# Kernel tuning notes

Measured on AMD Instinct MI355X. Metric: run time of the kernel, lower is better.

Reference implementation:

```python
import jax, jax.numpy as jnp
import numpy as np

H = 768        # bert hidden_size
HID = 512      # lstm_hidden
HALF = HID // 2
T = 20         # tagset_size
START, STOP = 18, 19
S = 16386      # input positions incl. CLS/SEP
NEG = -10000.0


def setup_inputs() -> dict:
    key = jax.random.key(0)
    ks = jax.random.split(key, 12)
    sc_x = 1.0
    x = jax.random.normal(ks[0], (1, S, H), dtype=jnp.float32)
    # PyTorch LSTM params (gate order i,f,g,o), one layer, bidirectional
    s_ih = 1.0 / np.sqrt(HALF)
    w_ih_f = jax.random.uniform(ks[1], (4 * HALF, H), jnp.float32, -s_ih, s_ih)
    w_hh_f = jax.random.uniform(ks[2], (4 * HALF, HALF), jnp.float32, -s_ih, s_ih)
    b_ih_f = jax.random.uniform(ks[3], (4 * HALF,), jnp.float32, -s_ih, s_ih)
    b_hh_f = jax.random.uniform(ks[4], (4 * HALF,), jnp.float32, -s_ih, s_ih)
    w_ih_b = jax.random.uniform(ks[5], (4 * HALF, H), jnp.float32, -s_ih, s_ih)
    w_hh_b = jax.random.uniform(ks[6], (4 * HALF, HALF), jnp.float32, -s_ih, s_ih)
    b_ih_b = jax.random.uniform(ks[7], (4 * HALF,), jnp.float32, -s_ih, s_ih)
    b_hh_b = jax.random.uniform(ks[8], (4 * HALF,), jnp.float32, -s_ih, s_ih)
    s_t = 1.0 / np.sqrt(HID)
    w_tag = jax.random.uniform(ks[9], (T, HID), jnp.float32, -s_t, s_t)
    b_tag = jax.random.uniform(ks[10], (T,), jnp.float32, -s_t, s_t)
    transitions = jax.random.normal(ks[11], (T, T), dtype=jnp.float32)
    transitions = transitions.at[START, :].set(NEG).at[:, STOP].set(NEG)
    return {
        "x": x,
        "w_ih_f": w_ih_f, "w_hh_f": w_hh_f, "b_ih_f": b_ih_f, "b_hh_f": b_hh_f,
        "w_ih_b": w_ih_b, "w_hh_b": w_hh_b, "b_ih_b": b_ih_b, "b_hh_b": b_hh_b,
        "w_tag": w_tag, "b_tag": b_tag, "transitions": transitions,
    }


def _lstm_one_step(xt, w_ih, b_ih, b_hh):
    # Original passes [1, N, H] to a batch_first=False LSTM => seq_len=1,
    # batch=N, zero initial state. So each token does ONE cell step:
    # h0=c0=0 => hh contribution is only b_hh.
    g = xt @ w_ih.T + b_ih + b_hh          # [N, 4*HALF]
    i, f, gg, o = jnp.split(g, 4, axis=-1)  # PyTorch gate order i,f,g,o
    c = jax.nn.sigmoid(i) * jnp.tanh(gg)    # f*c0 = 0
    return jax.nn.sigmoid(o) * jnp.tanh(c)  # [N, HALF]


def reference(x, w_ih_f, w_hh_f, b_ih_f, b_hh_f,
              w_ih_b, w_hh_b, b_ih_b, b_hh_b,
              w_tag, b_tag, transitions):
    tok = x[0, 1:-1, :]                     # narrow(1,1,S-2): drop CLS/SEP -> [N,H]
    h_f = _lstm_one_step(tok, w_ih_f, b_ih_f, b_hh_f)
    h_b = _lstm_one_step(tok, w_ih_b, b_ih_b, b_hh_b)
    enc = jnp.concatenate([h_f, h_b], axis=-1)   # [N, HID]
    feats = enc @ w_tag.T + b_tag                # [N, T] emission scores

    # ---- Viterbi decode (sequential DP over tokens) ----
    init = jnp.full((T,), NEG, dtype=feats.dtype).at[START].set(0.0)

    def vstep(fv, feat):
        scores = fv[None, :] + transitions       # [next_tag, prev_tag]
        bp = jnp.argmax(scores, axis=1)          # backpointers [T]
        fv_new = jnp.max(scores, axis=1) + feat
        return fv_new, bp

    fv, bps = jax.lax.scan(vstep, init, feats)   # bps: [N, T]
    terminal = fv + transitions[STOP]
    best = jnp.argmax(terminal)
    path_score = terminal[best]

    def btrack(b, bp):
        return bp[b], b                          # emit tag at time t, move to t-1

    _, best_path = jax.lax.scan(btrack, best, bps, reverse=True)  # [N] in time order
    return path_score, best_path
```

## Files before the change

### kernel.cpp

```cpp
#include <hip/hip_runtime.h>
#include <math.h>

#define HDIM 768
#define HIDD 512
#define NTOK 16384
#define NT 20
#define CHUNKS 128
#define CLEN 128

typedef unsigned short ushort_t;
typedef __attribute__((ext_vector_type(8))) short bf16x8;
typedef __attribute__((ext_vector_type(4))) float f32x4;

__device__ __forceinline__ float sigm(float x){ return 1.0f/(1.0f+expf(-x)); }

__device__ __forceinline__ ushort_t f2bf(float f){
    unsigned int u = __float_as_uint(f);
    unsigned int r = (u + 0x7fffu + ((u >> 16) & 1u)) >> 16;
    return (ushort_t)r;
}
__device__ __forceinline__ float bf2f(ushort_t b){
    return __uint_as_float(((unsigned int)b) << 16);
}

#define GLD16(gp, lp) __builtin_amdgcn_global_load_lds( \
    (const __attribute__((address_space(1))) void*)(gp), \
    (__attribute__((address_space(3))) void*)(lp), 16, 0, 0)

__global__ __launch_bounds__(256) void conv_kernel(
    const float* __restrict__ x,
    const float* __restrict__ wf, const float* __restrict__ wb,
    ushort_t* __restrict__ Ah, ushort_t* __restrict__ Al,
    ushort_t* __restrict__ Bh, ushort_t* __restrict__ Bl)
{
    const int bid = blockIdx.x;
    if (bid < 1152){
        int t = bid*256 + threadIdx.x;
        int n = t / 192, c4 = (t - n*192)*4;
        int dir = n / 768, nr = n - dir*768;
        int gate = nr >> 8, j = nr & 255;
        int wrow = j + ((gate==0)?0:((gate==1)?512:768));
        const float* src = dir ? wb : wf;
        const float4 v = *(const float4*)(src + (size_t)wrow*HDIM + c4);
        float f[4] = {v.x, v.y, v.z, v.w};
        ushort_t h[4], l[4];
        #pragma unroll
        for (int i=0;i<4;++i){
            h[i] = f2bf(f[i]);
            l[i] = f2bf(f[i] - bf2f(h[i]));
        }
        *(ushort4*)(Bh + (size_t)n*HDIM + c4) = make_ushort4(h[0],h[1],h[2],h[3]);
        *(ushort4*)(Bl + (size_t)n*HDIM + c4) = make_ushort4(l[0],l[1],l[2],l[3]);
    } else {
        int t = (bid-1152)*256 + threadIdx.x;
        int row = t / 192, c4 = (t - row*192)*4;
        const float4 v = *(const float4*)(x + (size_t)(row+1)*HDIM + c4);
        float f[4] = {v.x, v.y, v.z, v.w};
        ushort_t h[4], l[4];
        #pragma unroll
        for (int i=0;i<4;++i){
            h[i] = f2bf(f[i]);
            l[i] = f2bf(f[i] - bf2f(h[i]));
        }
        *(ushort4*)(Ah + (size_t)row*HDIM + c4) = make_ushort4(h[0],h[1],h[2],h[3]);
        *(ushort4*)(Al + (size_t)row*HDIM + c4) = make_ushort4(l[0],l[1],l[2],l[3]);
    }
}

#define VMCNT(n) asm volatile("s_waitcnt vmcnt(" #n ")" ::: "memory")
#define BARRIER() asm volatile("s_barrier" ::: "memory")

#define READ_B(S, g, ab) do{                                                  \
    bfr##S[0] = *(const bf16x8*)((ab) + 16384 + (g)*16384 + boffB[0]);        \
    bfr##S[1] = *(const bf16x8*)((ab) + 16384 + (g)*16384 + 8192 + boffB[0]); \
    bfr##S[2] = *(const bf16x8*)((ab) + 16384 + (g)*16384 + boffB[1]);        \
    bfr##S[3] = *(const bf16x8*)((ab) + 16384 + (g)*16384 + 8192 + boffB[1]); \
}while(0)

#define READ_A2(S, ab) do{ _Pragma("unroll") for (int f=0; f<4; ++f){         \
    aH##S[f] = *(const bf16x8*)((ab) + aoffB[f]);                             \
    aL##S[f] = *(const bf16x8*)((ab) + 8192 + aoffB[f]); } }while(0)

#define MFMA_CLUSTER(g, AS, BS) do{                                           \
  __builtin_amdgcn_sched_barrier(0);                                          \
  __builtin_amdgcn_s_setprio(1);                                              \
  _Pragma("unroll")                                                           \
  for (int fn=0; fn<2; ++fn){                                                 \
    _Pragma("unroll")                                                         \
    for (int fm=0; fm<4; ++fm){                                               \
      acc[g][fm][fn] = __builtin_amdgcn_mfma_f32_16x16x32_bf16(aH##AS[fm],    \
          bfr##BS[fn*2], acc[g][fm][fn], 0, 0, 0);                            \
      acc[g][fm][fn] = __builtin_amdgcn_mfma_f32_16x16x32_bf16(aL##AS[fm],    \
          bfr##BS[fn*2], acc[g][fm][fn], 0, 0, 0);                            \
      acc[g][fm][fn] = __builtin_amdgcn_mfma_f32_16x16x32_bf16(aH##AS[fm],    \
          bfr##BS[fn*2+1], acc[g][fm][fn], 0, 0, 0);                          \
    }                                                                         \
  }                                                                           \
  __builtin_amdgcn_s_setprio(0);                                              \
  __builtin_amdgcn_sched_barrier(0);                                          \
}while(0)

#define PH0(kt, P, AC, BC, BR) do{                                            \
    const int k0n = ((kt)+1)*32;                                              \
    char* abn = smem + (1-(P))*65536;                                         \
    const char* ab = smem + (P)*65536;                                        \
    VMCNT(2); BARRIER();                                                      \
    READ_B(BR, 1, ab);                                                        \
    GLD16(Ah + gA + k0n, abn + wbB);                                          \
    GLD16(Al + gA + k0n, abn + 8192 + wbB);                                   \
    GLD16(Bh + gB0 + k0n, abn + 16384 + wbB);                                 \
    GLD16(Bl + gB0 + k0n, abn + 24576 + wbB);                                 \
    MFMA_CLUSTER(0, AC, BC);                                                  \
}while(0)

#define PH1(kt, P, AC, BC, BR) do{                                            \
    const int k0n = ((kt)+1)*32;                                              \
    char* abn = smem + (1-(P))*65536;                                         \
    const char* ab = smem + (P)*65536;                                        \
    VMCNT(4); BARRIER();                                                      \
    READ_B(BR, 2, ab);                                                        \
    GLD16(Bh + gB1 + k0n, abn + 32768 + wbB);                                 \
    GLD16(Bl + gB1 + k0n, abn + 40960 + wbB);                                 \
    MFMA_CLUSTER(1, AC, BC);                                                  \
}while(0)

#define PH2(kt, P, AC, BC, BR, AN) do{                                        \
    const int k0n = ((kt)+1)*32;                                              \
    char* abn = smem + (1-(P))*65536;                                         \
    VMCNT(2); BARRIER();                                                      \
    READ_A2(AN, abn);                                                         \
    READ_B(BR, 0, abn);                                                       \
    GLD16(Bh + gB2 + k0n, abn + 49152 + wbB);                                 \
    GLD16(Bl + gB2 + k0n, abn + 57344 + wbB);                                 \
    MFMA_CLUSTER(2, AC, BC);                                                  \
}while(0)

__global__ __launch_bounds__(512, 2) void gemm_fused(
    const ushort_t* __restrict__ Ah, const ushort_t* __restrict__ Al,
    const ushort_t* __restrict__ Bh, const ushort_t* __restrict__ Bl,
    const float* __restrict__ bihf, const float* __restrict__ bhhf,
    const float* __restrict__ bihb, const float* __restrict__ bhhb,
    const float* __restrict__ wtag, float* __restrict__ featsp)
{
    __shared__ __align__(16) char smem[131072];
    float* hbuf = (float*)smem;
    float* wts  = (float*)(smem + 33280);

    const int tid = threadIdx.x;
    const int bx = blockIdx.x;
    const int xcd = bx & 7, g3 = bx >> 3;
    const int qb = g3 & 3, mt = (g3 >> 2)*8 + xcd;
    const int dir = qb >> 1, jhalf = qb & 1;
    const int j0 = jhalf*128;
    const int row0 = mt*128;
    const float* __restrict__ bih = dir ? bihb : bihf;
    const float* __restrict__ bhh = dir ? bhhb : bhhf;

    const int lane = tid & 63, wv = tid >> 6;
    const int wm = wv >> 2, wn = wv & 3;
    const int lm = lane & 15, lq = lane >> 4;
    const int wbB = (tid & 448) * 16;

    const int P_ = tid >> 3, s_ = tid & 7;
    const int q_ = s_ ^ (P_ & 7);
    const int mA = (P_ << 1) | (q_ >> 2);
    const int k8s = q_ & 3;
    const size_t gA  = (size_t)(row0 + mA)*HDIM + k8s*8;
    const size_t gB0 = (size_t)(dir*768 +           j0 + mA)*HDIM + k8s*8;
    const size_t gB1 = (size_t)(dir*768 + 256 +     j0 + mA)*HDIM + k8s*8;
    const size_t gB2 = (size_t)(dir*768 + 512 +     j0 + mA)*HDIM + k8s*8;

    int aoffB[4], boffB[2];
    #pragma unroll
    for (int f=0; f<4; ++f){
        int m = wm*64 + f*16 + lm;
        int rg = m >> 6, r = m & 63;
        aoffB[f] = rg*4096 + ((r>>1)*8 + ((((r&1)<<2)|lq) ^ ((r>>1)&7)))*16;
    }
    #pragma unroll
    for (int f=0; f<2; ++f){
        int n = wn*32 + f*16 + lm;
        int rg = n >> 6, r = n & 63;
        boffB[f] = rg*4096 + ((r>>1)*8 + ((((r&1)<<2)|lq) ^ ((r>>1)&7)))*16;
    }

    f32x4 acc[3][4][2];
    #pragma unroll
    for (int g=0; g<3; ++g)
        #pragma unroll
        for (int fm=0; fm<4; ++fm)
            #pragma unroll
            for (int fn=0; fn<2; ++fn)
                acc[g][fm][fn] = (f32x4){0.f,0.f,0.f,0.f};

    bf16x8 aH0[4], aL0[4], aH1[4], aL1[4];
    bf16x8 bfrA[4], bfrB[4];

    {
        GLD16(Ah + gA, smem + wbB);
        GLD16(Al + gA, smem + 8192 + wbB);
        GLD16(Bh + gB0, smem + 16384 + wbB);
        GLD16(Bl + gB0, smem + 24576 + wbB);
        GLD16(Bh + gB1, smem + 32768 + wbB);
        GLD16(Bl + gB1, smem + 40960 + wbB);
        GLD16(Bh + gB2, smem + 49152 + wbB);
        GLD16(Bl + gB2, smem + 57344 + wbB);
        VMCNT(4); BARRIER();
        READ_A2(0, (const char*)smem);
        READ_B(A, 0, (const char*)smem);
    }

    #pragma unroll 1
    for (int kt2 = 0; kt2 < 11; ++kt2){
        const int kt = kt2*2;
        PH0(kt,   0, 0, A, B); PH1(kt,   0, 0, B, A); PH2(kt,   0, 0, A, B, 1);
        PH0(kt+1, 1, 1, B, A); PH1(kt+1, 1, 1, A, B); PH2(kt+1, 1, 1, B, A, 0);
    }
    PH0(22, 0, 0, A, B); PH1(22, 0, 0, B, A); PH2(22, 0, 0, A, B, 1);

    {
        const char* ab = smem + 65536;
        VMCNT(2); BARRIER();
        READ_B(A, 1, ab);
        MFMA_CLUSTER(0, 1, B);
        VMCNT(0); BARRIER();
        READ_B(B, 2, ab);
        MFMA_CLUSTER(1, 1, A);
        MFMA_CLUSTER(2, 1, B);
    }

    int jcol[2];
    #pragma unroll
    for (int f=0; f<2; ++f) jcol[f] = j0 + wn*32 + f*16 + lm;

    float bi[2], bg_[2], bo[2];
    #pragma unroll
    for (int f=0; f<2; ++f){
        bi[f]  = bih[jcol[f]]       + bhh[jcol[f]];
        bg_[f] = bih[512 + jcol[f]] + bhh[512 + jcol[f]];
        bo[f]  = bih[768 + jcol[f]] + bhh[768 + jcol[f]];
    }
    float hv[4][2][4];
    #pragma unroll
    for (int fm=0; fm<4; ++fm)
        #pragma unroll
        for (int fn=0; fn<2; ++fn)
            #pragma unroll
            for (int r=0; r<4; ++r){
                float cv = sigm(acc[0][fm][fn][r] + bi[fn]) *
                           tanhf(acc[1][fm][fn][r] + bg_[fn]);
                hv[fm][fn][r] = sigm(acc[2][fm][fn][r] + bo[fn]) * tanhf(cv);
            }

    __syncthreads();
    for (int idx=tid; idx<2*NT*64; idx+=512){
        int cc = idx / (NT*64), r = idx - cc*(NT*64);
        int t = r >> 6, j = r & 63;
        wts[idx] = wtag[t*HIDD + dir*256 + j0 + cc*64 + j];
    }
    #pragma unroll 1
    for (int cc=0; cc<2; ++cc){
        __syncthreads();
        if ((wn >> 1) == cc){
            #pragma unroll
            for (int fm=0; fm<4; ++fm)
                #pragma unroll
                for (int fn=0; fn<2; ++fn)
                    #pragma unroll
                    for (int r=0; r<4; ++r){
                        int mloc = wm*64 + fm*16 + lq*4 + r;
                        int jloc = (wn&1)*32 + fn*16 + lm;
                        hbuf[mloc*65 + jloc] = hv[fm][fn][r];
                    }
        }
        __syncthreads();
        const int mrow = tid & 127, grp = tid >> 7;
        const int tg0 = grp*5;
        const float* wc = wts + cc*(NT*64);
        float s[5] = {0.f,0.f,0.f,0.f,0.f};
        for (int j=0;j<64;++j){
            float h = hbuf[mrow*65 + j];
            #pragma unroll
            for (int tt=0; tt<5; ++tt)
                s[tt] = fmaf(h, wc[(tg0+tt)*64 + j], s[tt]);
        }
        const int p = dir*4 + jhalf*2 + cc;
        float* fq = featsp + (size_t)p * (NTOK*NT);
        const int mglob = row0 + mrow;
        #pragma unroll
        for (int tt=0; tt<5; ++tt)
            fq[(size_t)mglob*NT + tg0 + tt] = s[tt];
    }
}

__device__ __forceinline__ void load_fl(
    const float* __restrict__ featsp, const float* __restrict__ btg,
    float* fl, int c, int tid, int nthr)
{
    const int base = c*(CLEN*NT/4);
    for (int idx=tid; idx<CLEN*NT/4; idx+=nthr){
        float4 s[8];
        #pragma unroll
        for (int p=0; p<8; ++p)
            s[p] = ((const float4*)(featsp + (size_t)p*NTOK*NT))[base+idx];
        float4 v;
        v.x = ((s[0].x+s[1].x)+(s[2].x+s[3].x)) + ((s[4].x+s[5].x)+(s[6].x+s[7].x));
        v.y = ((s[0].y+s[1].y)+(s[2].y+s[3].y)) + ((s[4].y+s[5].y)+(s[6].y+s[7].y));
        v.z = ((s[0].z+s[1].z)+(s[2].z+s[3].z)) + ((s[4].z+s[5].z)+(s[6].z+s[7].z));
        v.w = ((s[0].w+s[1].w)+(s[2].w+s[3].w)) + ((s[4].w+s[5].w)+(s[6].w+s[7].w));
        int t0 = (idx*4) % 20;
        v.x += btg[t0]; v.y += btg[t0+1]; v.z += btg[t0+2]; v.w += btg[t0+3];
        ((float4*)fl)[idx] = v;
    }
}

__global__ __launch_bounds__(256) void vit_chunkmat(
    const float* __restrict__ featsp, const float* __restrict__ btag,
    const float* __restrict__ trans, float* __restrict__ Pall)
{
    __shared__ float fl[CLEN*NT];
    __shared__ float Pt[2][NT*24];
    const int c = blockIdx.x, tid = threadIdx.x;
    load_fl(featsp, btag, fl, c, tid, 256);
    const bool act = tid < 200;
    const int j = tid / 10, ip = tid - j*10;
    const int ia = ip*2, ib = ia + 1;
    float tra[NT], trb[NT];
    if (act){
        #pragma unroll
        for (int k=0;k<NT;++k){
            tra[k] = trans[ia*NT+k];
            trb[k] = trans[ib*NT+k];
        }
        Pt[0][j*24+ia] = (ia==j) ? 0.f : -1e30f;
        Pt[0][j*24+ib] = (ib==j) ? 0.f : -1e30f;
    }
    __syncthreads();
    int cur = 0;
    #pragma unroll 1
    for (int t=0;t<CLEN;++t){
        if (act){
            float p[NT];
            #pragma unroll
            for (int q=0;q<5;++q){
                float4 v = *(const float4*)&Pt[cur][j*24 + q*4];
                p[q*4+0]=v.x; p[q*4+1]=v.y; p[q*4+2]=v.z; p[q*4+3]=v.w;
            }
            float ma = -3.0e38f, mb = -3.0e38f;
            #pragma unroll
            for (int k=0;k<NT;++k){
                ma = fmaxf(ma, tra[k] + p[k]);
                mb = fmaxf(mb, trb[k] + p[k]);
            }
            ma += fl[t*NT+ia];
            mb += fl[t*NT+ib];
            Pt[cur^1][j*24+ia] = ma;
            Pt[cur^1][j*24+ib] = mb;
        }
        __syncthreads();
        cur ^= 1;
    }
    if (act){
        Pall[(size_t)c*(NT*NT) + ia*NT + j] = Pt[cur][j*24+ia];
        Pall[(size_t)c*(NT*NT) + ib*NT + j] = Pt[cur][j*24+ib];
    }
}

__global__ __launch_bounds__(128) void vit_scan(
    const float* __restrict__ Pall, const float* __restrict__ trans,
    float* __restrict__ fvstart, float* __restrict__ dout, int* __restrict__ bestws)
{
    __shared__ float Pb[NT*NT];
    __shared__ float fv[NT];
    const int tid = threadIdx.x;
    float4 pn = {0.f,0.f,0.f,0.f};
    if (tid<100) pn = ((const float4*)Pall)[tid];
    if (tid<NT) fv[tid] = (tid==18) ? 0.f : -10000.f;
    for (int c=0;c<CHUNKS;++c){
        if (tid<100) ((float4*)Pb)[tid] = pn;
        if (tid<100 && c+1<CHUNKS) pn = ((const float4*)(Pall + (size_t)(c+1)*(NT*NT)))[tid];
        __syncthreads();
        if (tid<NT) fvstart[c*NT+tid] = fv[tid];
        float nf = -3.0e38f;
        if (tid<NT){
            #pragma unroll
            for (int j=0;j<NT;++j) nf = fmaxf(nf, Pb[tid*NT+j] + fv[j]);
        }
        __syncthreads();
        if (tid<NT) fv[tid] = nf;
    }
    __syncthreads();
    if (tid==0){
        float best = -3.0e38f; int bidx = 0;
        for (int j=0;j<NT;++j){
            float tv = fv[j] + trans[19*NT+j];
            if (tv > best){ best = tv; bidx = j; }
        }
        dout[0] = best;
        bestws[0] = bidx;
    }
}

__global__ __launch_bounds__(128) void vit_replay(
    const float* __restrict__ featsp, const float* __restrict__ btag,
    const float* __restrict__ trans, const float* __restrict__ fvstart,
    unsigned int* __restrict__ bpout, int* __restrict__ Hout)
{
    __shared__ float fl[CLEN*NT];
    __shared__ float fv[NT];
    __shared__ unsigned char bp[CLEN*NT];
    const int c = blockIdx.x, tid = threadIdx.x;
    load_fl(featsp, btag, fl, c, tid, 128);
    float tr[NT];
    if (tid<NT){
        fv[tid] = fvstart[c*NT+tid];
        #pragma unroll
        for (int k=0;k<NT;++k) tr[k] = trans[tid*NT+k];
    }
    __syncthreads();
    for (int t=0;t<CLEN;++t){
        float best = 0.f; int bj = 0;
        if (tid<NT){
            best = tr[0] + fv[0];
            #pragma unroll
            for (int j=1;j<NT;++j){
                float v = tr[j] + fv[j];
                if (v > best){ best = v; bj = j; }
            }
        }
        __syncthreads();
        if (tid<NT){
            fv[tid] = best + fl[t*NT+tid];
            bp[t*NT+tid] = (unsigned char)bj;
        }
        __syncthreads();
    }
    for (int idx=tid; idx<CLEN*NT/4; idx+=128)
        bpout[(size_t)c*(CLEN*NT/4) + idx] = ((unsigned int*)bp)[idx];
    if (tid<NT){
        int m = tid;
        for (int t=CLEN-1;t>=0;--t) m = bp[t*NT+m];
        Hout[c*NT+tid] = m;
    }
}

__global__ __launch_bounds__(64) void bt_fill(
    const unsigned int* __restrict__ bpin, const int* __restrict__ Hin,
    const int* __restrict__ bestws, float* __restrict__ dout)
{
    __shared__ int Hl[CHUNKS*NT];
    __shared__ unsigned char bp[CLEN*NT];
    __shared__ float ob[CLEN];
    const int c = blockIdx.x, tid = threadIdx.x;
    for (int idx=tid; idx<CHUNKS*NT; idx+=64) Hl[idx] = Hin[idx];
    for (int idx=tid; idx<CLEN*NT/4; idx+=64)
        ((unsigned int*)bp)[idx] = bpin[(size_t)c*(CLEN*NT/4) + idx];
    __syncthreads();
    if (tid==0){
        int e = bestws[0];
        for (int cc=CHUNKS-1; cc>c; --cc) e = Hl[cc*NT+e];
        for (int t=CLEN-1;t>=0;--t){ ob[t] = (float)e; e = bp[t*NT+e]; }
    }
    __syncthreads();
    for (int idx=tid; idx<CLEN; idx+=64)
        dout[1 + c*CLEN + idx] = ob[idx];
}

extern "C" void kernel_launch(void* const* d_in, const int* in_sizes, int n_in,
                              void* d_out, int out_size, void* d_ws, size_t ws_size,
                              hipStream_t stream)
{
    const float* x    = (const float*)d_in[0];
    const float* wf   = (const float*)d_in[1];
    const float* bihf = (const float*)d_in[3];
    const float* bhhf = (const float*)d_in[4];
    const float* wb   = (const float*)d_in[5];
    const float* bihb = (const float*)d_in[7];
    const float* bhhb = (const float*)d_in[8];
    const float* wtag = (const float*)d_in[9];
    const float* btag = (const float*)d_in[10];
    const float* trans= (const float*)d_in[11];
    float* out = (float*)d_out;

    char* w = (char*)d_ws;
    ushort_t* Ah = (ushort_t*)w;         w += 25165824;
    ushort_t* Al = (ushort_t*)w;         w += 25165824;
    ushort_t* Bh = (ushort_t*)w;         w += 2359296;
    ushort_t* Bl = (ushort_t*)w;         w += 2359296;
    float* featsp = (float*)w;           w += 10485760;
    float* Pall  = (float*)w;            w += 204800;
    float* fvst  = (float*)w;            w += 10240;
    int* Hmap    = (int*)w;              w += 10240;
    unsigned int* bp = (unsigned int*)w; w += 327680;
    int* best    = (int*)w;

    conv_kernel<<<13440, 256, 0, stream>>>(x, wf, wb, Ah, Al, Bh, Bl);
    gemm_fused<<<512, 512, 0, stream>>>(Ah, Al, Bh, Bl, bihf, bhhf, bihb, bhhb,
                                        wtag, featsp);
    vit_chunkmat<<<CHUNKS, 256, 0, stream>>>(featsp, btag, trans, Pall);
    vit_scan<<<1, 128, 0, stream>>>(Pall, trans, fvst, out, best);
    vit_replay<<<CHUNKS, 128, 0, stream>>>(featsp, btag, trans, fvst, bp, Hmap);
    bt_fill<<<CHUNKS, 64, 0, stream>>>(bp, Hmap, best, out);
}
```

Baseline: 366.9 us.

## Load GEMM B operand directly from global into registers, shrink LDS

The B (weight) fragments are now loaded straight from global memory into a register double buffer for the next k-step, instead of being staged through LDS with swizzled layouts. Only the A tile stays in LDS, so shared memory drops from 128KB to about 43KB and the per-phase barriers collapse into one wait-and-barrier per k-step. The aim is to cut LDS traffic and barrier count and to raise occupancy headroom. In exchange there are uncoalesced per-lane global reads of B, which are duplicated across the waves sharing a column slice, plus 24 extra bf16x8 registers. The full VMCNT(0) wait each step also removes the finer-grained overlap of the old schedule.

Result: slower. 503.1 us (+37.1%).

```diff
diff --git a/kernel.cpp b/kernel.cpp
--- a/kernel.cpp
+++ b/kernel.cpp
@@ -70,69 +70,48 @@
 #define VMCNT(n) asm volatile("s_waitcnt vmcnt(" #n ")" ::: "memory")
 #define BARRIER() asm volatile("s_barrier" ::: "memory")
 
-#define READ_B(S, g, ab) do{                                                  \
-    bfr##S[0] = *(const bf16x8*)((ab) + 16384 + (g)*16384 + boffB[0]);        \
-    bfr##S[1] = *(const bf16x8*)((ab) + 16384 + (g)*16384 + 8192 + boffB[0]); \
-    bfr##S[2] = *(const bf16x8*)((ab) + 16384 + (g)*16384 + boffB[1]);        \
-    bfr##S[3] = *(const bf16x8*)((ab) + 16384 + (g)*16384 + 8192 + boffB[1]); \
+#define LOADB(S, KT) do{                                                      \
+  _Pragma("unroll")                                                           \
+  for (int g=0; g<3; ++g)                                                     \
+    _Pragma("unroll")                                                         \
+    for (int f=0; f<2; ++f){                                                  \
+      bs##S[g*4+f*2+0] = *(const bf16x8*)((const char*)Bh + bByte[g][f] + (KT)*64); \
+      bs##S[g*4+f*2+1] = *(const bf16x8*)((const char*)Bl + bByte[g][f] + (KT)*64); \
+    }                                                                         \
 }while(0)
 
-#define READ_A2(S, ab) do{ _Pragma("unroll") for (int f=0; f<4; ++f){         \
-    aH##S[f] = *(const bf16x8*)((ab) + aoffB[f]);                             \
-    aL##S[f] = *(const bf16x8*)((ab) + 8192 + aoffB[f]); } }while(0)
-
-#define MFMA_CLUSTER(g, AS, BS) do{                                           \
+#define READ_A(ab) do{ _Pragma("unroll") for (int f=0; f<4; ++f){             \
+    aH[f] = *(const bf16x8*)((ab) + aoffB[f]);                                \
+    aL[f] = *(const bf16x8*)((ab) + 8192 + aoffB[f]); } }while(0)
+
+#define MFMA_CLUSTER(g, S) do{                                                \
   __builtin_amdgcn_sched_barrier(0);                                          \
   __builtin_amdgcn_s_setprio(1);                                              \
   _Pragma("unroll")                                                           \
   for (int fn=0; fn<2; ++fn){                                                 \
     _Pragma("unroll")                                                         \
     for (int fm=0; fm<4; ++fm){                                               \
-      acc[g][fm][fn] = __builtin_amdgcn_mfma_f32_16x16x32_bf16(aH##AS[fm],    \
-          bfr##BS[fn*2], acc[g][fm][fn], 0, 0, 0);                            \
-      acc[g][fm][fn] = __builtin_amdgcn_mfma_f32_16x16x32_bf16(aL##AS[fm],    \
-          bfr##BS[fn*2], acc[g][fm][fn], 0, 0, 0);                            \
-      acc[g][fm][fn] = __builtin_amdgcn_mfma_f32_16x16x32_bf16(aH##AS[fm],    \
-          bfr##BS[fn*2+1], acc[g][fm][fn], 0, 0, 0);                          \
+      acc[g][fm][fn] = __builtin_amdgcn_mfma_f32_16x16x32_bf16(aH[fm],        \
+          bs##S[(g)*4+fn*2], acc[g][fm][fn], 0, 0, 0);                        \
+      acc[g][fm][fn] = __builtin_amdgcn_mfma_f32_16x16x32_bf16(aL[fm],        \
+          bs##S[(g)*4+fn*2], acc[g][fm][fn], 0, 0, 0);                        \
+      acc[g][fm][fn] = __builtin_amdgcn_mfma_f32_16x16x32_bf16(aH[fm],        \
+          bs##S[(g)*4+fn*2+1], acc[g][fm][fn], 0, 0, 0);                      \
     }                                                                         \
   }                                                                           \
   __builtin_amdgcn_s_setprio(0);                                              \
   __builtin_amdgcn_sched_barrier(0);                                          \
 }while(0)
 
-#define PH0(kt, P, AC, BC, BR) do{                                            \
-    const int k0n = ((kt)+1)*32;                                              \
-    char* abn = smem + (1-(P))*65536;                                         \
-    const char* ab = smem + (P)*65536;                                        \
-    VMCNT(2); BARRIER();                                                      \
-    READ_B(BR, 1, ab);                                                        \
-    GLD16(Ah + gA + k0n, abn + wbB);                                          \
-    GLD16(Al + gA + k0n, abn + 8192 + wbB);                                   \
-    GLD16(Bh + gB0 + k0n, abn + 16384 + wbB);                                 \
-    GLD16(Bl + gB0 + k0n, abn + 24576 + wbB);                                 \
-    MFMA_CLUSTER(0, AC, BC);                                                  \
-}while(0)
-
-#define PH1(kt, P, AC, BC, BR) do{                                            \
-    const int k0n = ((kt)+1)*32;                                              \
-    char* abn = smem + (1-(P))*65536;                                         \
-    const char* ab = smem + (P)*65536;                                        \
-    VMCNT(4); BARRIER();                                                      \
-    READ_B(BR, 2, ab);                                                        \
-    GLD16(Bh + gB1 + k0n, abn + 32768 + wbB);                                 \
-    GLD16(Bl + gB1 + k0n, abn + 40960 + wbB);                                 \
-    MFMA_CLUSTER(1, AC, BC);                                                  \
-}while(0)
-
-#define PH2(kt, P, AC, BC, BR, AN) do{                                        \
-    const int k0n = ((kt)+1)*32;                                              \
-    char* abn = smem + (1-(P))*65536;                                         \
-    VMCNT(2); BARRIER();                                                      \
-    READ_A2(AN, abn);                                                         \
-    READ_B(BR, 0, abn);                                                       \
-    GLD16(Bh + gB2 + k0n, abn + 49152 + wbB);                                 \
-    GLD16(Bl + gB2 + k0n, abn + 57344 + wbB);                                 \
-    MFMA_CLUSTER(2, AC, BC);                                                  \
+#define KT_BODY(KT, P, CUR, NXT) do{                                          \
+    VMCNT(0); BARRIER();                                                      \
+    READ_A(smem + (P)*16384);                                                 \
+    LOADB(NXT, (KT)+1);                                                       \
+    GLD16(Ah + gA + ((KT)+1)*32, smem + (1-(P))*16384 + wbB);                 \
+    GLD16(Al + gA + ((KT)+1)*32, smem + (1-(P))*16384 + 8192 + wbB);          \
+    MFMA_CLUSTER(0, CUR);                                                     \
+    MFMA_CLUSTER(1, CUR);                                                     \
+    MFMA_CLUSTER(2, CUR);                                                     \
 }while(0)
 
 __global__ __launch_bounds__(512, 2) void gemm_fused(
@@ -142,7 +121,7 @@
     const float* __restrict__ bihb, const float* __restrict__ bhhb,
     const float* __restrict__ wtag, float* __restrict__ featsp)
 {
-    __shared__ __align__(16) char smem[131072];
+    __shared__ __align__(16) char smem[43520];
     float* hbuf = (float*)smem;
     float* wts  = (float*)(smem + 33280);
 
@@ -166,23 +145,22 @@
     const int mA = (P_ << 1) | (q_ >> 2);
     const int k8s = q_ & 3;
     const size_t gA  = (size_t)(row0 + mA)*HDIM + k8s*8;
-    const size_t gB0 = (size_t)(dir*768 +           j0 + mA)*HDIM + k8s*8;
-    const size_t gB1 = (size_t)(dir*768 + 256 +     j0 + mA)*HDIM + k8s*8;
-    const size_t gB2 = (size_t)(dir*768 + 512 +     j0 + mA)*HDIM + k8s*8;
-
-    int aoffB[4], boffB[2];
+
+    int aoffB[4];
     #pragma unroll
     for (int f=0; f<4; ++f){
         int m = wm*64 + f*16 + lm;
         int rg = m >> 6, r = m & 63;
         aoffB[f] = rg*4096 + ((r>>1)*8 + ((((r&1)<<2)|lq) ^ ((r>>1)&7)))*16;
     }
-    #pragma unroll
-    for (int f=0; f<2; ++f){
-        int n = wn*32 + f*16 + lm;
-        int rg = n >> 6, r = n & 63;
-        boffB[f] = rg*4096 + ((r>>1)*8 + ((((r&1)<<2)|lq) ^ ((r>>1)&7)))*16;
-    }
+
+    int bByte[3][2];
+    #pragma unroll
+    for (int g=0; g<3; ++g)
+        #pragma unroll
+        for (int f=0; f<2; ++f)
+            bByte[g][f] = (dir*768 + g*256 + j0 + wn*32 + f*16 + lm)*(HDIM*2)
+                          + lq*16;
 
     f32x4 acc[3][4][2];
     #pragma unroll
@@ -193,40 +171,26 @@
             for (int fn=0; fn<2; ++fn)
                 acc[g][fm][fn] = (f32x4){0.f,0.f,0.f,0.f};
 
-    bf16x8 aH0[4], aL0[4], aH1[4], aL1[4];
-    bf16x8 bfrA[4], bfrB[4];
-
-    {
-        GLD16(Ah + gA, smem + wbB);
-        GLD16(Al + gA, smem + 8192 + wbB);
-        GLD16(Bh + gB0, smem + 16384 + wbB);
-        GLD16(Bl + gB0, smem + 24576 + wbB);
-        GLD16(Bh + gB1, smem + 32768 + wbB);
-        GLD16(Bl + gB1, smem + 40960 + wbB);
-        GLD16(Bh + gB2, smem + 49152 + wbB);
-        GLD16(Bl + gB2, smem + 57344 + wbB);
-        VMCNT(4); BARRIER();
-        READ_A2(0, (const char*)smem);
-        READ_B(A, 0, (const char*)smem);
-    }
+    bf16x8 aH[4], aL[4];
+    bf16x8 bsA[12], bsB[12];
+
+    LOADB(A, 0);
+    GLD16(Ah + gA, smem + wbB);
+    GLD16(Al + gA, smem + 8192 + wbB);
 
     #pragma unroll 1
     for (int kt2 = 0; kt2 < 11; ++kt2){
-        const int kt = kt2*2;
-        PH0(kt,   0, 0, A, B); PH1(kt,   0, 0, B, A); PH2(kt,   0, 0, A, B, 1);
-        PH0(kt+1, 1, 1, B, A); PH1(kt+1, 1, 1, A, B); PH2(kt+1, 1, 1, B, A, 0);
-    }
-    PH0(22, 0, 0, A, B); PH1(22, 0, 0, B, A); PH2(22, 0, 0, A, B, 1);
+        KT_BODY(2*kt2,   0, A, B);
+        KT_BODY(2*kt2+1, 1, B, A);
+    }
+    KT_BODY(22, 0, A, B);
 
     {
-        const char* ab = smem + 65536;
-        VMCNT(2); BARRIER();
-        READ_B(A, 1, ab);
-        MFMA_CLUSTER(0, 1, B);
         VMCNT(0); BARRIER();
-        READ_B(B, 2, ab);
-        MFMA_CLUSTER(1, 1, A);
-        MFMA_CLUSTER(2, 1, B);
+        READ_A(smem + 16384);
+        MFMA_CLUSTER(0, B);
+        MFMA_CLUSTER(1, B);
+        MFMA_CLUSTER(2, B);
     }
 
     int jcol[2];
```
